# Kernel optimization log

Measured on AMD Instinct MI355X. Metric: run time of the kernel, lower is better.

Reference implementation:

```python
import jax, jax.numpy as jnp
import numpy as np

NUM_HEADS = 8
DIM_HEAD = 128
SCALE = DIM_HEAD ** -0.5


def setup_inputs() -> dict:
    key = jax.random.key(0)
    ks = jax.random.split(key, 6)
    B, N, D = 8, 1024, 1024
    return {
        "s_v": jax.random.normal(ks[0], (B, N, D), jnp.float32),
        "s_m": jax.random.normal(ks[1], (B, N, D), jnp.float32),
        "g_l": jax.random.normal(ks[2], (B, NUM_HEADS, N, N), jnp.float32),
        "W_qkv": jax.random.normal(ks[3], (D, 3 * NUM_HEADS * DIM_HEAD), jnp.float32) * (D ** -0.5),
        "W_qk": jax.random.normal(ks[4], (D, 2 * NUM_HEADS * DIM_HEAD), jnp.float32) * (D ** -0.5),
        "W_out": jax.random.normal(ks[5], (NUM_HEADS * DIM_HEAD, D), jnp.float32) * ((NUM_HEADS * DIM_HEAD) ** -0.5),
        "b_out": jnp.zeros((D,), jnp.float32),
    }


def _split_heads(t):
    # [b, n, h*d] -> [b, h, n, d]
    b, n, hd = t.shape
    return t.reshape(b, n, NUM_HEADS, DIM_HEAD).transpose(0, 2, 1, 3)


def reference(s_v, s_m, g_l, W_qkv, W_qk, W_out, b_out):
    b, n, _ = s_v.shape
    q_v, k_v, v = [_split_heads(t) for t in jnp.split(s_v @ W_qkv, 3, axis=-1)]
    q_m, k_m = [_split_heads(t) for t in jnp.split(s_m @ W_qk, 2, axis=-1)]
    # trajectory attention probs (softmaxed) times raw value-stream scores
    p_m = jax.nn.softmax(jnp.einsum('bhid,bhjd->bhij', q_m, k_m), axis=-1)
    p_v = jnp.einsum('bhid,bhjd->bhij', q_v, k_v)
    dots = p_m * p_v * SCALE + g_l
    attn = jax.nn.softmax(dots, axis=-1)
    out = jnp.einsum('bhij,bhjd->bhid', attn, v)
    out = out.transpose(0, 2, 1, 3).reshape(b, n, NUM_HEADS * DIM_HEAD)
    return out @ W_out + b_out
```

## Files before the change

### kernel.cpp

```cpp
#include <hip/hip_runtime.h>

typedef __attribute__((ext_vector_type(8))) short short8;
typedef __attribute__((ext_vector_type(8))) unsigned short ushortx8;
typedef __attribute__((ext_vector_type(4))) unsigned short ushortx4;
typedef __attribute__((ext_vector_type(4))) float floatx4;

#define SCALE_F 0.08838834764831845f

__device__ __forceinline__ float b2f(unsigned short u) {
  union { unsigned int u; float f; } c; c.u = ((unsigned int)u) << 16; return c.f;
}
__device__ __forceinline__ unsigned short f2b(float f) {
  union { float f; unsigned int u; } c; c.f = f;
  unsigned int u = c.u;
  u += 0x7fffu + ((u >> 16) & 1u);
  return (unsigned short)(u >> 16);
}

#define GLD_LDS16(g, l)                                              \
  __builtin_amdgcn_global_load_lds(                                  \
      (const __attribute__((address_space(1))) void*)(g),            \
      (__attribute__((address_space(3))) void*)(l), 16, 0, 0)

__global__ __launch_bounds__(256) void cast_bf16_kernel(
    const float* __restrict__ x, unsigned short* __restrict__ y, int n) {
  int i = (blockIdx.x * 256 + threadIdx.x) * 4;
  if (i >= n) return;
  float4 v = *(const float4*)(x + i);
  ushortx4 o;
  o[0] = f2b(v.x); o[1] = f2b(v.y); o[2] = f2b(v.z); o[3] = f2b(v.w);
  *(ushortx4*)(y + i) = o;
}

__global__ __launch_bounds__(256) void split2_kernel(
    const float* __restrict__ x, unsigned short* __restrict__ y) {
  int idx = blockIdx.x * 256 + threadIdx.x;
  int row = idx >> 8;
  int c4 = (idx & 255) * 4;
  float4 v = *(const float4*)(x + (size_t)row * 1024 + c4);
  ushortx4 hi, lo;
  hi[0] = f2b(v.x); lo[0] = f2b(v.x - b2f(hi[0]));
  hi[1] = f2b(v.y); lo[1] = f2b(v.y - b2f(hi[1]));
  hi[2] = f2b(v.z); lo[2] = f2b(v.z - b2f(hi[2]));
  hi[3] = f2b(v.w); lo[3] = f2b(v.w - b2f(hi[3]));
  unsigned short* yr = y + (size_t)row * 2048;
  *(ushortx4*)(yr + c4) = hi;
  *(ushortx4*)(yr + 1024 + c4) = lo;
}

__global__ __launch_bounds__(256) void transpose_split_qk(
    const float* __restrict__ W, unsigned short* __restrict__ y) {
  __shared__ float tile[32][33];
  int t = threadIdx.x, tx = t & 31, ty = t >> 5;
  int n0 = blockIdx.x * 32, k0 = blockIdx.y * 32;
  for (int rr = ty; rr < 32; rr += 8)
    tile[rr][tx] = W[(size_t)(k0 + rr) * 2048 + n0 + tx];
  __syncthreads();
  for (int rr = ty; rr < 32; rr += 8) {
    float v = tile[tx][rr];
    unsigned short hi = f2b(v);
    unsigned short* yr = y + (size_t)(n0 + rr) * 2048;
    yr[k0 + tx] = hi;
    yr[1024 + k0 + tx] = hi;
  }
}

template<int MODE>
__global__ __launch_bounds__(256) void transpose_any(
    const void* __restrict__ inv, void* __restrict__ outv,
    int R, int C, int ldin, int ldout,
    long sIb, long sIh, long sOb, long sOh, int pstart) {
  int z = blockIdx.z, p = pstart + z, b = p >> 3, h = p & 7;
  size_t ioff = (size_t)(sIb * b + sIh * h);
  size_t ooff = (size_t)(sOb * b + sOh * h);
  __shared__ float tile[32][33];
  int t = threadIdx.x, tx = t & 31, ty = t >> 5;
  int c0 = blockIdx.x * 32, r0 = blockIdx.y * 32;
  for (int rr = ty; rr < 32; rr += 8) {
    size_t idx = ioff + (size_t)(r0 + rr) * ldin + (c0 + tx);
    tile[rr][tx] = (MODE == 2) ? b2f(((const unsigned short*)inv)[idx])
                               : ((const float*)inv)[idx];
  }
  __syncthreads();
  for (int rr = ty; rr < 32; rr += 8) {
    size_t idx = ooff + (size_t)(c0 + rr) * ldout + (r0 + tx);
    ((unsigned short*)outv)[idx] = f2b(tile[tx][rr]);
  }
}

template<int OUT_BF16, int ADD_BIAS>
__global__ __launch_bounds__(256) void gemm128(
    const unsigned short* __restrict__ A, const unsigned short* __restrict__ BT,
    void* __restrict__ Cv, const float* __restrict__ bias,
    int K, int lda, int ldb, int ldc,
    long sAz, long sAb, long sAh, long sBz, long sBb, long sBh,
    long sCz, long sCb, long sCh, int pstart) {
  int z = blockIdx.z, p = pstart + z, bb = p >> 3, hh = p & 7;
  A  += (size_t)(sAz * z + sAb * bb + sAh * hh);
  BT += (size_t)(sBz * z + sBb * bb + sBh * hh);
  size_t coff = (size_t)(sCz * z + sCb * bb + sCh * hh);

  __shared__ unsigned short Al[128][32];
  __shared__ unsigned short Bl[128][32];
  int t = threadIdx.x;
  int m0 = blockIdx.y * 128, n0 = blockIdx.x * 128;
  int w = t >> 6, l = t & 63;
  int wm = (w >> 1) * 64, wn = (w & 1) * 64;
  int lrow = l & 15, lq = l >> 4;
  floatx4 acc[4][4] = {};

  int srow = t >> 2, scol = (t & 3) * 8;
  const unsigned short* ga = A + (size_t)(m0 + srow) * lda + scol;
  const unsigned short* gb = BT + (size_t)(n0 + srow) * ldb + scol;
  unsigned short* la = &Al[srow][scol];
  unsigned short* lb = &Bl[srow][scol];
  size_t lda64 = (size_t)64 * lda, ldb64 = (size_t)64 * ldb;

  for (int k0 = 0; k0 < K; k0 += 32) {
    GLD_LDS16(ga + k0, la);
    GLD_LDS16(ga + lda64 + k0, la + 64 * 32);
    GLD_LDS16(gb + k0, lb);
    GLD_LDS16(gb + ldb64 + k0, lb + 64 * 32);
    __syncthreads();
    short8 af[4], bf[4];
#pragma unroll
    for (int i = 0; i < 4; i++) af[i] = *(const short8*)&Al[wm + i * 16 + lrow][lq * 8];
#pragma unroll
    for (int j = 0; j < 4; j++) bf[j] = *(const short8*)&Bl[wn + j * 16 + lrow][lq * 8];
#pragma unroll
    for (int i = 0; i < 4; i++)
#pragma unroll
      for (int j = 0; j < 4; j++)
        acc[i][j] = __builtin_amdgcn_mfma_f32_16x16x32_bf16(af[i], bf[j], acc[i][j], 0, 0, 0);
    __syncthreads();
  }
#pragma unroll
  for (int i = 0; i < 4; i++)
#pragma unroll
    for (int j = 0; j < 4; j++)
#pragma unroll
      for (int r = 0; r < 4; r++) {
        int row = m0 + wm + i * 16 + lq * 4 + r;
        int col = n0 + wn + j * 16 + lrow;
        float v = acc[i][j][r];
        if (ADD_BIAS) v += bias[col];
        size_t idx = coff + (size_t)row * ldc + col;
        if (OUT_BF16) ((unsigned short*)Cv)[idx] = f2b(v);
        else          ((float*)Cv)[idx] = v;
      }
}

template<int OUT_BF16, int ADD_BIAS>
__global__ __launch_bounds__(256) void gemm64(
    const unsigned short* __restrict__ A, const unsigned short* __restrict__ BT,
    void* __restrict__ Cv, const float* __restrict__ bias,
    int K, int lda, int ldb, int ldc,
    long sAz, long sAb, long sAh, long sBz, long sBb, long sBh,
    long sCz, long sCb, long sCh, int pstart) {
  int z = blockIdx.z, p = pstart + z, bb = p >> 3, hh = p & 7;
  A  += (size_t)(sAz * z + sAb * bb + sAh * hh);
  BT += (size_t)(sBz * z + sBb * bb + sBh * hh);
  size_t coff = (size_t)(sCz * z + sCb * bb + sCh * hh);

  __shared__ unsigned short Al[64][32];
  __shared__ unsigned short Bl[128][32];
  int t = threadIdx.x;
  int m0 = blockIdx.y * 64, n0 = blockIdx.x * 128;
  int w = t >> 6, l = t & 63;
  int wm = (w >> 1) * 32, wn = (w & 1) * 64;
  int lrow = l & 15, lq = l >> 4;
  floatx4 acc[2][4] = {};

  int srow = t >> 2, scol = (t & 3) * 8;
  const unsigned short* ga = A + (size_t)(m0 + srow) * lda + scol;
  const unsigned short* gb = BT + (size_t)(n0 + srow) * ldb + scol;
  unsigned short* la = &Al[srow][scol];
  unsigned short* lb = &Bl[srow][scol];
  size_t ldb64 = (size_t)64 * ldb;

  for (int k0 = 0; k0 < K; k0 += 32) {
    GLD_LDS16(ga + k0, la);
    GLD_LDS16(gb + k0, lb);
    GLD_LDS16(gb + ldb64 + k0, lb + 64 * 32);
    __syncthreads();
    short8 af[2], bf[4];
#pragma unroll
    for (int i = 0; i < 2; i++) af[i] = *(const short8*)&Al[wm + i * 16 + lrow][lq * 8];
#pragma unroll
    for (int j = 0; j < 4; j++) bf[j] = *(const short8*)&Bl[wn + j * 16 + lrow][lq * 8];
#pragma unroll
    for (int i = 0; i < 2; i++)
#pragma unroll
      for (int j = 0; j < 4; j++)
        acc[i][j] = __builtin_amdgcn_mfma_f32_16x16x32_bf16(af[i], bf[j], acc[i][j], 0, 0, 0);
    __syncthreads();
  }
#pragma unroll
  for (int i = 0; i < 2; i++)
#pragma unroll
    for (int j = 0; j < 4; j++)
#pragma unroll
      for (int r = 0; r < 4; r++) {
        int row = m0 + wm + i * 16 + lq * 4 + r;
        int col = n0 + wn + j * 16 + lrow;
        float v = acc[i][j][r];
        if (ADD_BIAS) v += bias[col];
        size_t idx = coff + (size_t)row * ldc + col;
        if (OUT_BF16) ((unsigned short*)Cv)[idx] = f2b(v);
        else          ((float*)Cv)[idx] = v;
      }
}

__global__ __launch_bounds__(256) void logits_prep(
    const float* __restrict__ qkf, unsigned short* __restrict__ qm,
    unsigned short* __restrict__ km, int pstart) {
  int idx = blockIdx.x * 256 + threadIdx.x;
  int z = blockIdx.y;
  int i = idx >> 5;
  int d4 = (idx & 31) * 4;
  int p = pstart + z, b = p >> 3, h = p & 7;
  const float* row = qkf + ((size_t)(b * 1024 + i)) * 2048 + h * 128;
  ushortx4 hi, lo;

  float4 q = *(const float4*)(row + d4);
  hi[0] = f2b(q.x); lo[0] = f2b(q.x - b2f(hi[0]));
  hi[1] = f2b(q.y); lo[1] = f2b(q.y - b2f(hi[1]));
  hi[2] = f2b(q.z); lo[2] = f2b(q.z - b2f(hi[2]));
  hi[3] = f2b(q.w); lo[3] = f2b(q.w - b2f(hi[3]));
  unsigned short* qr = qm + ((size_t)z * 1024 + i) * 384;
  *(ushortx4*)(qr + d4) = hi;
  *(ushortx4*)(qr + 128 + d4) = lo;
  *(ushortx4*)(qr + 256 + d4) = hi;

  float4 k = *(const float4*)(row + 1024 + d4);
  hi[0] = f2b(k.x); lo[0] = f2b(k.x - b2f(hi[0]));
  hi[1] = f2b(k.y); lo[1] = f2b(k.y - b2f(hi[1]));
  hi[2] = f2b(k.z); lo[2] = f2b(k.z - b2f(hi[2]));
  hi[3] = f2b(k.w); lo[3] = f2b(k.w - b2f(hi[3]));
  unsigned short* kr = km + ((size_t)z * 1024 + i) * 384;
  *(ushortx4*)(kr + d4) = hi;
  *(ushortx4*)(kr + 128 + d4) = hi;
  *(ushortx4*)(kr + 256 + d4) = lo;
}

__global__ __launch_bounds__(256) void softmax_combine(
    const float* __restrict__ smb, unsigned short* __restrict__ pvb,
    const float* __restrict__ g_l, int pstart) {
  int z = blockIdx.y, p = pstart + z;
  int w = threadIdx.x >> 6, l = threadIdx.x & 63;
  int i = blockIdx.x * 4 + w;
  const float* srow = smb + ((size_t)z * 1024 + i) * 1024;
  unsigned short* vrow = pvb + ((size_t)z * 1024 + i) * 1024;
  const float* grow = g_l + ((size_t)p * 1024 + i) * 1024;

  float4 s[4];
#pragma unroll
  for (int j = 0; j < 4; j++) s[j] = *(const float4*)(srow + j * 256 + l * 4);
  float mx = -3.0e38f;
#pragma unroll
  for (int j = 0; j < 4; j++)
    mx = fmaxf(mx, fmaxf(fmaxf(s[j].x, s[j].y), fmaxf(s[j].z, s[j].w)));
#pragma unroll
  for (int o = 32; o; o >>= 1) mx = fmaxf(mx, __shfl_xor(mx, o));
  float sum = 0.0f;
#pragma unroll
  for (int j = 0; j < 4; j++) {
    s[j].x = __expf(s[j].x - mx); s[j].y = __expf(s[j].y - mx);
    s[j].z = __expf(s[j].z - mx); s[j].w = __expf(s[j].w - mx);
    sum += (s[j].x + s[j].y) + (s[j].z + s[j].w);
  }
#pragma unroll
  for (int o = 32; o; o >>= 1) sum += __shfl_xor(sum, o);
  float inv = 1.0f / sum;

  float4 d[4];
#pragma unroll
  for (int j = 0; j < 4; j++) {
    ushortx4 pv = *(const ushortx4*)(vrow + j * 256 + l * 4);
    float4 g = *(const float4*)(grow + j * 256 + l * 4);
    d[j].x = s[j].x * inv * b2f(pv[0]) * SCALE_F + g.x;
    d[j].y = s[j].y * inv * b2f(pv[1]) * SCALE_F + g.y;
    d[j].z = s[j].z * inv * b2f(pv[2]) * SCALE_F + g.z;
    d[j].w = s[j].w * inv * b2f(pv[3]) * SCALE_F + g.w;
  }
  float mx2 = -3.0e38f;
#pragma unroll
  for (int j = 0; j < 4; j++)
    mx2 = fmaxf(mx2, fmaxf(fmaxf(d[j].x, d[j].y), fmaxf(d[j].z, d[j].w)));
#pragma unroll
  for (int o = 32; o; o >>= 1) mx2 = fmaxf(mx2, __shfl_xor(mx2, o));
  float sum2 = 0.0f;
#pragma unroll
  for (int j = 0; j < 4; j++) {
    d[j].x = __expf(d[j].x - mx2); d[j].y = __expf(d[j].y - mx2);
    d[j].z = __expf(d[j].z - mx2); d[j].w = __expf(d[j].w - mx2);
    sum2 += (d[j].x + d[j].y) + (d[j].z + d[j].w);
  }
#pragma unroll
  for (int o = 32; o; o >>= 1) sum2 += __shfl_xor(sum2, o);
  float inv2 = 1.0f / sum2;

#pragma unroll
  for (int j = 0; j < 4; j++) {
    ushortx4 o4;
    o4[0] = f2b(d[j].x * inv2); o4[1] = f2b(d[j].y * inv2);
    o4[2] = f2b(d[j].z * inv2); o4[3] = f2b(d[j].w * inv2);
    *(ushortx4*)(vrow + j * 256 + l * 4) = o4;
  }
}

extern "C" void kernel_launch(void* const* d_in, const int* in_sizes, int n_in,
                              void* d_out, int out_size, void* d_ws, size_t ws_size,
                              hipStream_t stream) {
  (void)in_sizes; (void)n_in; (void)out_size;
  const float* s_v   = (const float*)d_in[0];
  const float* s_m   = (const float*)d_in[1];
  const float* g_l   = (const float*)d_in[2];
  const float* W_qkv = (const float*)d_in[3];
  const float* W_qk  = (const float*)d_in[4];
  const float* W_out = (const float*)d_in[5];
  const float* b_out = (const float*)d_in[6];
  float* out = (float*)d_out;
  char* ws = (char*)d_ws;

  const bool big = (ws_size >= (size_t)721420288ull);

  unsigned short *sv_bf, *qm384, *km384, *wtqkv, *wtout, *qkvb, *vt, *ao,
                 *smhl, *wqk_hl, *pvb;
  float *qkf, *smb;
  if (big) {
    sv_bf  = (unsigned short*)(ws);
    wtqkv  = (unsigned short*)(ws + 16777216);
    wtout  = (unsigned short*)(ws + 23068672);
    qkvb   = (unsigned short*)(ws + 25165824);
    qkf    = (float*)         (ws + 75497472);
    vt     = (unsigned short*)(ws + 142606336);
    ao     = (unsigned short*)(ws + 159383552);
    smhl   = (unsigned short*)(ws + 176160768);
    wqk_hl = (unsigned short*)(ws + 209715200);
    qm384  = (unsigned short*)(ws + 218103808);
    km384  = (unsigned short*)(ws + 268435456);
    smb    = (float*)         (ws + 318767104);
    pvb    = (unsigned short*)(ws + 587202560);
  } else {
    sv_bf  = (unsigned short*)(ws);
    qm384  = (unsigned short*)(ws);
    wtqkv  = (unsigned short*)(ws + 16777216);
    km384  = (unsigned short*)(ws + 16777216);
    wtout  = (unsigned short*)(ws + 29360128);
    qkvb   = (unsigned short*)(ws + 31457280);
    qkf    = (float*)         (ws + 81788928);
    vt     = (unsigned short*)(ws + 148897792);
    ao     = (unsigned short*)(ws + 165675008);
    smhl   = (unsigned short*)(ws + 182452224);
    smb    = (float*)         (ws + 182452224);
    wqk_hl = (unsigned short*)(ws + 249561088);
    pvb    = (unsigned short*)(ws + 249561088);
  }

  cast_bf16_kernel<<<dim3(8192), 256, 0, stream>>>(s_v, sv_bf, 8388608);
  transpose_any<0><<<dim3(96, 32, 1), 256, 0, stream>>>(
      W_qkv, wtqkv, 1024, 3072, 3072, 1024, 0, 0, 0, 0, 0);
  transpose_any<0><<<dim3(32, 32, 1), 256, 0, stream>>>(
      W_out, wtout, 1024, 1024, 1024, 1024, 0, 0, 0, 0, 0);
  split2_kernel<<<dim3(8192), 256, 0, stream>>>(s_m, smhl);
  transpose_split_qk<<<dim3(64, 32, 1), 256, 0, stream>>>(W_qk, wqk_hl);
  gemm128<1, 0><<<dim3(24, 64, 1), 256, 0, stream>>>(
      sv_bf, wtqkv, qkvb, nullptr, 1024, 1024, 1024, 3072,
      0, 0, 0, 0, 0, 0, 0, 0, 0, 0);
  gemm128<0, 0><<<dim3(16, 64, 1), 256, 0, stream>>>(
      smhl, wqk_hl, qkf, nullptr, 2048, 2048, 2048, 2048,
      0, 0, 0, 0, 0, 0, 0, 0, 0, 0);
  transpose_any<2><<<dim3(4, 32, 64), 256, 0, stream>>>(
      qkvb + 2048, vt, 1024, 128, 3072, 1024,
      (long)1024 * 3072, 128, (long)1048576, 131072, 0);

  if (big) {
    logits_prep<<<dim3(128, 64), 256, 0, stream>>>(qkf, qm384, km384, 0);
    gemm128<0, 0><<<dim3(8, 8, 64), 256, 0, stream>>>(
        qm384, km384, smb, nullptr, 384, 384, 384, 1024,
        (long)1024 * 384, 0, 0, (long)1024 * 384, 0, 0,
        (long)1048576, 0, 0, 0);
    gemm128<1, 0><<<dim3(8, 8, 64), 256, 0, stream>>>(
        qkvb, qkvb + 1024, pvb, nullptr, 128, 3072, 3072, 1024,
        0, (long)1024 * 3072, 128, 0, (long)1024 * 3072, 128,
        (long)1048576, 0, 0, 0);
    softmax_combine<<<dim3(256, 64), 256, 0, stream>>>(smb, pvb, g_l, 0);
    gemm128<1, 0><<<dim3(1, 8, 64), 256, 0, stream>>>(
        pvb, vt, ao, nullptr, 1024, 1024, 1024, 1024,
        (long)1048576, 0, 0, 0, (long)1048576, 131072,
        0, (long)1048576, 128, 0);
  } else {
    for (int c = 0; c < 4; c++) {
      int pstart = c * 16;
      logits_prep<<<dim3(128, 16), 256, 0, stream>>>(qkf, qm384, km384, pstart);
      gemm128<0, 0><<<dim3(8, 8, 16), 256, 0, stream>>>(
          qm384, km384, smb, nullptr, 384, 384, 384, 1024,
          (long)1024 * 384, 0, 0, (long)1024 * 384, 0, 0,
          (long)1048576, 0, 0, pstart);
      gemm128<1, 0><<<dim3(8, 8, 16), 256, 0, stream>>>(
          qkvb, qkvb + 1024, pvb, nullptr, 128, 3072, 3072, 1024,
          0, (long)1024 * 3072, 128, 0, (long)1024 * 3072, 128,
          (long)1048576, 0, 0, pstart);
      softmax_combine<<<dim3(256, 16), 256, 0, stream>>>(smb, pvb, g_l, pstart);
      gemm64<1, 0><<<dim3(1, 16, 16), 256, 0, stream>>>(
          pvb, vt, ao, nullptr, 1024, 1024, 1024, 1024,
          (long)1048576, 0, 0, 0, (long)1048576, 131072,
          0, (long)1048576, 128, pstart);
    }
  }
  gemm128<0, 1><<<dim3(8, 64, 1), 256, 0, stream>>>(
      ao, wtout, out, b_out, 1024, 1024, 1024, 1024,
      0, 0, 0, 0, 0, 0, 0, 0, 0, 0);
}
```

Measured before the change: 1.018 ms.

## Fuse double softmax with attention-times-V MFMA into one kernel

Adds a softmax_av kernel. For each block it computes the two-stage softmax for 16 query rows, stores the bf16 probabilities in swizzled LDS, then multiplies them by V^T with double-buffered global-to-LDS loads and bf16 MFMA, writing the head output directly. The goal is to skip writing the full attention matrix to global memory and reading it back for a separate GEMM. The cost is a narrow 16-row M tile, so V^T is re-read once per row block and each block gets less MFMA work. The launch order in the large-workspace path is also shuffled, moving the q_v·k_v GEMM ahead of the s_m projection GEMM.

```diff
diff --git a/kernel.cpp b/kernel.cpp
--- a/kernel.cpp
+++ b/kernel.cpp
@@ -307,6 +307,127 @@
     o4[2] = f2b(d[j].z * inv2); o4[3] = f2b(d[j].w * inv2);
     *(ushortx4*)(vrow + j * 256 + l * 4) = o4;
   }
+}
+
+__global__ __launch_bounds__(256) void softmax_av(
+    const float* __restrict__ smb, const unsigned short* __restrict__ pvb,
+    const float* __restrict__ g_l, const unsigned short* __restrict__ vt,
+    unsigned short* __restrict__ ao, int pstart) {
+  int z = blockIdx.y, p = pstart + z, b = p >> 3, h = p & 7;
+  int m0 = blockIdx.x * 16;
+  int t = threadIdx.x, w = t >> 6, l = t & 63;
+
+  __shared__ unsigned short attn[16 * 1024];
+  __shared__ unsigned short Bl[2][128][32];
+
+  const unsigned short* BT = vt + (size_t)p * 131072;
+  int srow = t >> 2, scol = (t & 3) * 8;
+  const unsigned short* gb = BT + (size_t)srow * 1024 + scol;
+  GLD_LDS16(gb, &Bl[0][srow][scol]);
+  GLD_LDS16(gb + 64 * 1024, &Bl[0][srow + 64][scol]);
+
+  for (int it = 0; it < 4; it++) {
+    int r = it * 4 + w;
+    int i = m0 + r;
+    const float* srw = smb + ((size_t)z * 1024 + i) * 1024;
+    const unsigned short* vrow = pvb + ((size_t)z * 1024 + i) * 1024;
+    const float* grow = g_l + ((size_t)p * 1024 + i) * 1024;
+
+    float4 s[4];
+#pragma unroll
+    for (int j = 0; j < 4; j++) s[j] = *(const float4*)(srw + j * 256 + l * 4);
+    float mx = -3.0e38f;
+#pragma unroll
+    for (int j = 0; j < 4; j++)
+      mx = fmaxf(mx, fmaxf(fmaxf(s[j].x, s[j].y), fmaxf(s[j].z, s[j].w)));
+#pragma unroll
+    for (int o = 32; o; o >>= 1) mx = fmaxf(mx, __shfl_xor(mx, o));
+    float sum = 0.0f;
+#pragma unroll
+    for (int j = 0; j < 4; j++) {
+      s[j].x = __expf(s[j].x - mx); s[j].y = __expf(s[j].y - mx);
+      s[j].z = __expf(s[j].z - mx); s[j].w = __expf(s[j].w - mx);
+      sum += (s[j].x + s[j].y) + (s[j].z + s[j].w);
+    }
+#pragma unroll
+    for (int o = 32; o; o >>= 1) sum += __shfl_xor(sum, o);
+    float inv = 1.0f / sum;
+
+    float4 d[4];
+#pragma unroll
+    for (int j = 0; j < 4; j++) {
+      ushortx4 pv = *(const ushortx4*)(vrow + j * 256 + l * 4);
+      float4 g = *(const float4*)(grow + j * 256 + l * 4);
+      d[j].x = s[j].x * inv * b2f(pv[0]) * SCALE_F + g.x;
+      d[j].y = s[j].y * inv * b2f(pv[1]) * SCALE_F + g.y;
+      d[j].z = s[j].z * inv * b2f(pv[2]) * SCALE_F + g.z;
+      d[j].w = s[j].w * inv * b2f(pv[3]) * SCALE_F + g.w;
+    }
+    float mx2 = -3.0e38f;
+#pragma unroll
+    for (int j = 0; j < 4; j++)
+      mx2 = fmaxf(mx2, fmaxf(fmaxf(d[j].x, d[j].y), fmaxf(d[j].z, d[j].w)));
+#pragma unroll
+    for (int o = 32; o; o >>= 1) mx2 = fmaxf(mx2, __shfl_xor(mx2, o));
+    float sum2 = 0.0f;
+#pragma unroll
+    for (int j = 0; j < 4; j++) {
+      d[j].x = __expf(d[j].x - mx2); d[j].y = __expf(d[j].y - mx2);
+      d[j].z = __expf(d[j].z - mx2); d[j].w = __expf(d[j].w - mx2);
+      sum2 += (d[j].x + d[j].y) + (d[j].z + d[j].w);
+    }
+#pragma unroll
+    for (int o = 32; o; o >>= 1) sum2 += __shfl_xor(sum2, o);
+    float inv2 = 1.0f / sum2;
+
+    unsigned sw = (unsigned)(r & 7) << 4;
+    char* base = (char*)attn + r * 2048;
+#pragma unroll
+    for (int j = 0; j < 4; j++) {
+      ushortx4 o4;
+      o4[0] = f2b(d[j].x * inv2); o4[1] = f2b(d[j].y * inv2);
+      o4[2] = f2b(d[j].z * inv2); o4[3] = f2b(d[j].w * inv2);
+      *(ushortx4*)(base + ((unsigned)(j * 512 + l * 8) ^ sw)) = o4;
+    }
+  }
+  __syncthreads();
+
+  int wn = w * 32;
+  int lrow = l & 15, lq = l >> 4;
+  floatx4 acc[2] = {};
+
+  unsigned arow = (unsigned)lrow;
+  unsigned abase = arow * 2048;
+  unsigned asw = (arow & 7) << 4;
+
+  for (int ks = 0; ks < 32; ks++) {
+    int cur = ks & 1;
+    if (ks < 31) {
+      const unsigned short* gn = gb + (ks + 1) * 32;
+      GLD_LDS16(gn, &Bl[cur ^ 1][srow][scol]);
+      GLD_LDS16(gn + 64 * 1024, &Bl[cur ^ 1][srow + 64][scol]);
+    }
+    short8 af = *(const short8*)((char*)attn + abase +
+                                 ((unsigned)(ks * 64 + lq * 16) ^ asw));
+    short8 bf[2];
+#pragma unroll
+    for (int j = 0; j < 2; j++)
+      bf[j] = *(const short8*)&Bl[cur][wn + j * 16 + lrow][lq * 8];
+#pragma unroll
+    for (int j = 0; j < 2; j++)
+      acc[j] = __builtin_amdgcn_mfma_f32_16x16x32_bf16(af, bf[j], acc[j], 0, 0, 0);
+    __syncthreads();
+  }
+
+  size_t coff = (size_t)b * 1048576 + (size_t)h * 128;
+#pragma unroll
+  for (int j = 0; j < 2; j++)
+#pragma unroll
+    for (int r4 = 0; r4 < 4; r4++) {
+      int row = m0 + lq * 4 + r4;
+      int col = wn + j * 16 + lrow;
+      ao[coff + (size_t)row * 1024 + col] = f2b(acc[j][r4]);
+    }
 }
 
 extern "C" void kernel_launch(void* const* d_in, const int* in_sizes, int n_in,
@@ -368,29 +489,28 @@
   gemm128<1, 0><<<dim3(24, 64, 1), 256, 0, stream>>>(
       sv_bf, wtqkv, qkvb, nullptr, 1024, 1024, 1024, 3072,
       0, 0, 0, 0, 0, 0, 0, 0, 0, 0);
-  gemm128<0, 0><<<dim3(16, 64, 1), 256, 0, stream>>>(
-      smhl, wqk_hl, qkf, nullptr, 2048, 2048, 2048, 2048,
-      0, 0, 0, 0, 0, 0, 0, 0, 0, 0);
   transpose_any<2><<<dim3(4, 32, 64), 256, 0, stream>>>(
       qkvb + 2048, vt, 1024, 128, 3072, 1024,
       (long)1024 * 3072, 128, (long)1048576, 131072, 0);
 
   if (big) {
+    gemm128<1, 0><<<dim3(8, 8, 64), 256, 0, stream>>>(
+        qkvb, qkvb + 1024, pvb, nullptr, 128, 3072, 3072, 1024,
+        0, (long)1024 * 3072, 128, 0, (long)1024 * 3072, 128,
+        (long)1048576, 0, 0, 0);
+    gemm128<0, 0><<<dim3(16, 64, 1), 256, 0, stream>>>(
+        smhl, wqk_hl, qkf, nullptr, 2048, 2048, 2048, 2048,
+        0, 0, 0, 0, 0, 0, 0, 0, 0, 0);
     logits_prep<<<dim3(128, 64), 256, 0, stream>>>(qkf, qm384, km384, 0);
     gemm128<0, 0><<<dim3(8, 8, 64), 256, 0, stream>>>(
         qm384, km384, smb, nullptr, 384, 384, 384, 1024,
         (long)1024 * 384, 0, 0, (long)1024 * 384, 0, 0,
         (long)1048576, 0, 0, 0);
-    gemm128<1, 0><<<dim3(8, 8, 64), 256, 0, stream>>>(
-        qkvb, qkvb + 1024, pvb, nullptr, 128, 3072, 3072, 1024,
-        0, (long)1024 * 3072, 128, 0, (long)1024 * 3072, 128,
-        (long)1048576, 0, 0, 0);
-    softmax_combine<<<dim3(256, 64), 256, 0, stream>>>(smb, pvb, g_l, 0);
-    gemm128<1, 0><<<dim3(1, 8, 64), 256, 0, stream>>>(
-        pvb, vt, ao, nullptr, 1024, 1024, 1024, 1024,
-        (long)1048576, 0, 0, 0, (long)1048576, 131072,
-        0, (long)1048576, 128, 0);
+    softmax_av<<<dim3(64, 64), 256, 0, stream>>>(smb, pvb, g_l, vt, ao, 0);
   } else {
+    gemm128<0, 0><<<dim3(16, 64, 1), 256, 0, stream>>>(
+        smhl, wqk_hl, qkf, nullptr, 2048, 2048, 2048, 2048,
+        0, 0, 0, 0, 0, 0, 0, 0, 0, 0);
     for (int c = 0; c < 4; c++) {
       int pstart = c * 16;
       logits_prep<<<dim3(128, 16), 256, 0, stream>>>(qkf, qm384, km384, pstart);
```

New measurement: 1.018 ms. About the same (+0.0%).

## Fuse dual-softmax attention into a single per-row-block kernel

Applied to the files above, without the earlier changes.

Replaces the big-workspace path's separate kernels (score GEMMs for both streams, softmax_combine, and the attn@V GEMM) with one fused kernel. Each 512-thread block handles 16 query rows of one head: it computes both score tiles with MFMA, does both softmaxes using cross-wave reductions in LDS, stages the bf16 probabilities in swizzled LDS, and multiplies by V^T. This avoids writing and re-reading the full fp32/bf16 N×N intermediates in global memory. The cost is re-reading K tiles from global for every 16-row block and a large LDS footprint that limits occupancy.

```diff
diff --git a/kernel.cpp b/kernel.cpp
--- a/kernel.cpp
+++ b/kernel.cpp
@@ -1,7 +1,6 @@
 #include <hip/hip_runtime.h>
 
 typedef __attribute__((ext_vector_type(8))) short short8;
-typedef __attribute__((ext_vector_type(8))) unsigned short ushortx8;
 typedef __attribute__((ext_vector_type(4))) unsigned short ushortx4;
 typedef __attribute__((ext_vector_type(4))) float floatx4;
 
@@ -306,6 +305,237 @@
     o4[0] = f2b(d[j].x * inv2); o4[1] = f2b(d[j].y * inv2);
     o4[2] = f2b(d[j].z * inv2); o4[3] = f2b(d[j].w * inv2);
     *(ushortx4*)(vrow + j * 256 + l * 4) = o4;
+  }
+}
+
+__global__ __launch_bounds__(512, 4) void fused_attn(
+    const unsigned short* __restrict__ qm384, const unsigned short* __restrict__ km384,
+    const unsigned short* __restrict__ qkvb, const unsigned short* __restrict__ vt,
+    const float* __restrict__ g_l, unsigned short* __restrict__ ao) {
+  int z = blockIdx.y, b = z >> 3, h = z & 7;
+  int m0 = blockIdx.x * 16;
+  int t = threadIdx.x, w = t >> 6, l = t & 63;
+  int lrow = l & 15, lq = l >> 4;
+
+  __shared__ unsigned short attnL[16 * 1024];
+  __shared__ unsigned short qmL[16 * 384];
+  __shared__ unsigned short qvL[16 * 128];
+  __shared__ float red[4][8][16];
+
+  const char* qmg = (const char*)(qm384 + (size_t)z * 393216 + (size_t)m0 * 384);
+  const char* qvg = (const char*)(qkvb + (size_t)b * 3145728 + (size_t)m0 * 3072 + h * 128);
+  {
+    unsigned o = (unsigned)t * 16;
+    unsigned r = o / 768, c = o % 768;
+    GLD_LDS16(qmg + r * 768 + (c ^ ((r & 7) << 4)), (char*)qmL + o);
+    unsigned s = (unsigned)t + 512;
+    if (s < 768) {
+      o = s * 16; r = o / 768; c = o % 768;
+      GLD_LDS16(qmg + r * 768 + (c ^ ((r & 7) << 4)), (char*)qmL + o);
+    } else {
+      unsigned o2 = (s - 768) * 16;
+      unsigned r2 = o2 / 256, c2 = o2 % 256;
+      GLD_LDS16(qvg + r2 * 6144 + (c2 ^ ((r2 & 7) << 4)), (char*)qvL + o2);
+    }
+  }
+
+  const float* gp = g_l + (size_t)z * 1048576 +
+                    (size_t)(m0 + lq * 4) * 1024 + w * 128 + lrow;
+  float g0[4][4];
+#pragma unroll
+  for (int tc = 0; tc < 4; tc++)
+#pragma unroll
+    for (int r4 = 0; r4 < 4; r4++)
+      g0[tc][r4] = gp[(size_t)r4 * 1024 + tc * 16];
+
+  __syncthreads();
+
+  const unsigned short* kvg = qkvb + (size_t)b * 3145728 + 1024 + h * 128;
+  floatx4 pacc[8];
+#pragma unroll
+  for (int tc = 0; tc < 8; tc++) pacc[tc] = (floatx4){0.f, 0.f, 0.f, 0.f};
+  unsigned qvsw = ((unsigned)lrow & 7) << 4;
+#pragma unroll
+  for (int k0 = 0; k0 < 4; k0++) {
+    short8 af = *(const short8*)((char*)qvL + lrow * 256 +
+                                 ((unsigned)(k0 * 64 + lq * 16) ^ qvsw));
+#pragma unroll
+    for (int tc = 0; tc < 8; tc++) {
+      int col = w * 128 + tc * 16 + lrow;
+      short8 bf = *(const short8*)(kvg + (size_t)col * 3072 + k0 * 32 + lq * 8);
+      pacc[tc] = __builtin_amdgcn_mfma_f32_16x16x32_bf16(af, bf, pacc[tc], 0, 0, 0);
+    }
+  }
+  unsigned pvp[8][2];
+#pragma unroll
+  for (int tc = 0; tc < 8; tc++)
+#pragma unroll
+    for (int j = 0; j < 2; j++)
+      pvp[tc][j] = (unsigned)f2b(pacc[tc][2 * j]) |
+                   ((unsigned)f2b(pacc[tc][2 * j + 1]) << 16);
+
+  const unsigned short* kmg = km384 + (size_t)z * 393216;
+  floatx4 sacc[8];
+#pragma unroll
+  for (int tc = 0; tc < 8; tc++) sacc[tc] = (floatx4){0.f, 0.f, 0.f, 0.f};
+#pragma unroll
+  for (int k0 = 0; k0 < 12; k0++) {
+    short8 af = *(const short8*)((char*)qmL + lrow * 768 +
+                                 ((unsigned)(k0 * 64 + lq * 16) ^ qvsw));
+#pragma unroll
+    for (int tc = 0; tc < 8; tc++) {
+      int col = w * 128 + tc * 16 + lrow;
+      short8 bf = *(const short8*)(kmg + (size_t)col * 384 + k0 * 32 + lq * 8);
+      sacc[tc] = __builtin_amdgcn_mfma_f32_16x16x32_bf16(af, bf, sacc[tc], 0, 0, 0);
+    }
+  }
+
+  float g1[4][4];
+#pragma unroll
+  for (int tc = 0; tc < 4; tc++)
+#pragma unroll
+    for (int r4 = 0; r4 < 4; r4++)
+      g1[tc][r4] = gp[(size_t)r4 * 1024 + (tc + 4) * 16];
+
+  float m1[4];
+#pragma unroll
+  for (int r4 = 0; r4 < 4; r4++) {
+    float mx = sacc[0][r4];
+#pragma unroll
+    for (int tc = 1; tc < 8; tc++) mx = fmaxf(mx, sacc[tc][r4]);
+#pragma unroll
+    for (int o = 1; o < 16; o <<= 1) mx = fmaxf(mx, __shfl_xor(mx, o));
+    m1[r4] = mx;
+  }
+  if (lrow == 0) {
+#pragma unroll
+    for (int r4 = 0; r4 < 4; r4++) red[0][w][lq * 4 + r4] = m1[r4];
+  }
+  __syncthreads();
+#pragma unroll
+  for (int r4 = 0; r4 < 4; r4++) {
+    float mx = red[0][0][lq * 4 + r4];
+#pragma unroll
+    for (int ww = 1; ww < 8; ww++) mx = fmaxf(mx, red[0][ww][lq * 4 + r4]);
+    m1[r4] = mx;
+  }
+  float s1[4] = {0.f, 0.f, 0.f, 0.f};
+#pragma unroll
+  for (int tc = 0; tc < 8; tc++)
+#pragma unroll
+    for (int r4 = 0; r4 < 4; r4++) {
+      float e = __expf(sacc[tc][r4] - m1[r4]);
+      sacc[tc][r4] = e;
+      s1[r4] += e;
+    }
+#pragma unroll
+  for (int r4 = 0; r4 < 4; r4++) {
+#pragma unroll
+    for (int o = 1; o < 16; o <<= 1) s1[r4] += __shfl_xor(s1[r4], o);
+  }
+  if (lrow == 0) {
+#pragma unroll
+    for (int r4 = 0; r4 < 4; r4++) red[1][w][lq * 4 + r4] = s1[r4];
+  }
+  __syncthreads();
+  float inv1[4];
+#pragma unroll
+  for (int r4 = 0; r4 < 4; r4++) {
+    float sm = red[1][0][lq * 4 + r4];
+#pragma unroll
+    for (int ww = 1; ww < 8; ww++) sm += red[1][ww][lq * 4 + r4];
+    inv1[r4] = 1.0f / sm;
+  }
+
+#pragma unroll
+  for (int tc = 0; tc < 8; tc++)
+#pragma unroll
+    for (int r4 = 0; r4 < 4; r4++) {
+      float pv = b2f((unsigned short)(pvp[tc][r4 >> 1] >> ((r4 & 1) * 16)));
+      float gg = (tc < 4) ? g0[tc][r4] : g1[tc - 4][r4];
+      sacc[tc][r4] = sacc[tc][r4] * inv1[r4] * pv * SCALE_F + gg;
+    }
+
+  float m2[4];
+#pragma unroll
+  for (int r4 = 0; r4 < 4; r4++) {
+    float mx = sacc[0][r4];
+#pragma unroll
+    for (int tc = 1; tc < 8; tc++) mx = fmaxf(mx, sacc[tc][r4]);
+#pragma unroll
+    for (int o = 1; o < 16; o <<= 1) mx = fmaxf(mx, __shfl_xor(mx, o));
+    m2[r4] = mx;
+  }
+  if (lrow == 0) {
+#pragma unroll
+    for (int r4 = 0; r4 < 4; r4++) red[2][w][lq * 4 + r4] = m2[r4];
+  }
+  __syncthreads();
+#pragma unroll
+  for (int r4 = 0; r4 < 4; r4++) {
+    float mx = red[2][0][lq * 4 + r4];
+#pragma unroll
+    for (int ww = 1; ww < 8; ww++) mx = fmaxf(mx, red[2][ww][lq * 4 + r4]);
+    m2[r4] = mx;
+  }
+  float s2[4] = {0.f, 0.f, 0.f, 0.f};
+#pragma unroll
+  for (int tc = 0; tc < 8; tc++)
+#pragma unroll
+    for (int r4 = 0; r4 < 4; r4++) {
+      float e = __expf(sacc[tc][r4] - m2[r4]);
+      sacc[tc][r4] = e;
+      s2[r4] += e;
+    }
+#pragma unroll
+  for (int r4 = 0; r4 < 4; r4++) {
+#pragma unroll
+    for (int o = 1; o < 16; o <<= 1) s2[r4] += __shfl_xor(s2[r4], o);
+  }
+  if (lrow == 0) {
+#pragma unroll
+    for (int r4 = 0; r4 < 4; r4++) red[3][w][lq * 4 + r4] = s2[r4];
+  }
+  __syncthreads();
+  float inv2[4];
+#pragma unroll
+  for (int r4 = 0; r4 < 4; r4++) {
+    float sm = red[3][0][lq * 4 + r4];
+#pragma unroll
+    for (int ww = 1; ww < 8; ww++) sm += red[3][ww][lq * 4 + r4];
+    inv2[r4] = 1.0f / sm;
+  }
+
+#pragma unroll
+  for (int tc = 0; tc < 8; tc++)
+#pragma unroll
+    for (int r4 = 0; r4 < 4; r4++) {
+      int row = lq * 4 + r4;
+      unsigned col = (unsigned)(w * 128 + tc * 16 + lrow);
+      unsigned byte = (unsigned)(row * 2048 + col * 2) ^ (((unsigned)row & 7) << 4);
+      *(unsigned short*)((char*)attnL + byte) = f2b(sacc[tc][r4] * inv2[r4]);
+    }
+  __syncthreads();
+
+  const unsigned short* BT = vt + (size_t)z * 131072;
+  floatx4 acc = {};
+  unsigned abase = (unsigned)lrow * 2048;
+  unsigned asw = ((unsigned)lrow & 7) << 4;
+  const unsigned short* b0 = BT + (size_t)(w * 16 + lrow) * 1024 + lq * 8;
+#pragma unroll 4
+  for (int ks = 0; ks < 32; ks++) {
+    short8 af = *(const short8*)((char*)attnL + abase +
+                                 ((unsigned)(ks * 64 + lq * 16) ^ asw));
+    short8 bf = *(const short8*)(b0 + ks * 32);
+    acc = __builtin_amdgcn_mfma_f32_16x16x32_bf16(af, bf, acc, 0, 0, 0);
+  }
+
+  size_t coff = (size_t)b * 1048576 + (size_t)h * 128;
+#pragma unroll
+  for (int r4 = 0; r4 < 4; r4++) {
+    int row = m0 + lq * 4 + r4;
+    int col = w * 16 + lrow;
+    ao[coff + (size_t)row * 1024 + col] = f2b(acc[r4]);
   }
 }
 
@@ -368,28 +598,16 @@
   gemm128<1, 0><<<dim3(24, 64, 1), 256, 0, stream>>>(
       sv_bf, wtqkv, qkvb, nullptr, 1024, 1024, 1024, 3072,
       0, 0, 0, 0, 0, 0, 0, 0, 0, 0);
+  transpose_any<2><<<dim3(4, 32, 64), 256, 0, stream>>>(
+      qkvb + 2048, vt, 1024, 128, 3072, 1024,
+      (long)1024 * 3072, 128, (long)1048576, 131072, 0);
   gemm128<0, 0><<<dim3(16, 64, 1), 256, 0, stream>>>(
       smhl, wqk_hl, qkf, nullptr, 2048, 2048, 2048, 2048,
       0, 0, 0, 0, 0, 0, 0, 0, 0, 0);
-  transpose_any<2><<<dim3(4, 32, 64), 256, 0, stream>>>(
-      qkvb + 2048, vt, 1024, 128, 3072, 1024,
-      (long)1024 * 3072, 128, (long)1048576, 131072, 0);
 
   if (big) {
     logits_prep<<<dim3(128, 64), 256, 0, stream>>>(qkf, qm384, km384, 0);
-    gemm128<0, 0><<<dim3(8, 8, 64), 256, 0, stream>>>(
-        qm384, km384, smb, nullptr, 384, 384, 384, 1024,
-        (long)1024 * 384, 0, 0, (long)1024 * 384, 0, 0,
-        (long)1048576, 0, 0, 0);
-    gemm128<1, 0><<<dim3(8, 8, 64), 256, 0, stream>>>(
-        qkvb, qkvb + 1024, pvb, nullptr, 128, 3072, 3072, 1024,
-        0, (long)1024 * 3072, 128, 0, (long)1024 * 3072, 128,
-        (long)1048576, 0, 0, 0);
-    softmax_combine<<<dim3(256, 64), 256, 0, stream>>>(smb, pvb, g_l, 0);
-    gemm128<1, 0><<<dim3(1, 8, 64), 256, 0, stream>>>(
-        pvb, vt, ao, nullptr, 1024, 1024, 1024, 1024,
-        (long)1048576, 0, 0, 0, (long)1048576, 131072,
-        0, (long)1048576, 128, 0);
+    fused_attn<<<dim3(64, 64), 512, 0, stream>>>(qm384, km384, qkvb, vt, g_l, ao);
   } else {
     for (int c = 0; c < 4; c++) {
       int pstart = c * 16;
```

New measurement: 1.321 ms. 29.7% more time.
